# Kernel optimization log

Hardware: AMD Instinct MI355X
Metric: run time of the kernel (lower is better)

The kernel has to match this reference:

```python
import jax, jax.numpy as jnp
import numpy as np
import math

V, D, H, NH, T, S = 50257, 1024, 1024, 16, 128, 4096
HD = D // NH


def setup_inputs() -> dict:
    key = jax.random.key(0)
    ks = jax.random.split(key, 24)
    sc = 0.02

    def n(k, shape, scale=sc):
        return jax.random.normal(k, shape, dtype=jnp.float32) * scale

    return {
        "sentence": jax.random.randint(ks[0], (S,), 0, V),
        "emb": n(ks[1], (V, D), 1.0),
        # attention projections, stored as (in, out) = W.T of torch Linear
        "Wq": n(ks[2], (D, D)), "bq": jnp.zeros((D,), jnp.float32),
        "Wk": n(ks[3], (D, D)), "bk": jnp.zeros((D,), jnp.float32),
        "Wv": n(ks[4], (D, D)), "bv": jnp.zeros((D,), jnp.float32),
        "Wo": n(ks[5], (D, D)), "bo": jnp.zeros((D,), jnp.float32),
        # LSTM gate linears: (D+H, H) each
        "Wf": n(ks[6], (D + H, H)), "bf": jnp.zeros((H,), jnp.float32),
        "Wi": n(ks[7], (D + H, H)), "bi": jnp.zeros((H,), jnp.float32),
        "Wu": n(ks[8], (D + H, H)), "bu": jnp.zeros((H,), jnp.float32),
        "Wg": n(ks[9], (D + H, H)), "bg": jnp.zeros((H,), jnp.float32),
        # tagger
        "Wt": n(ks[10], (H, T)), "bt": jnp.zeros((T,), jnp.float32),
    }


def _forward(sentence, emb, Wq, bq, Wk, bk, Wv, bv, Wo, bo,
             Wf, bf, Wi, bi, Wu, bu, Wg, bg, Wt, bt):
    s = sentence.shape[0]
    x = emb[sentence]                       # [S, D] embedding gather
    h = x[:, None, :]                       # [S, 1, D]  (seq, batch, embed)

    # Faithful to the torch code: scores contract over the BATCH axis
    # (view(seq, batch, heads, hd).transpose(1, 2) -> (seq, heads, batch, hd)).
    def proj(W, b):
        return (h @ W + b).reshape(s, 1, NH, HD).transpose(0, 2, 1, 3)  # [S,NH,1,HD]

    q, k, v = proj(Wq, bq), proj(Wk, bk), proj(Wv, bv)
    scores = jnp.einsum('shbd,shcd->shbc', q, k) / math.sqrt(HD)  # [S,NH,1,1]
    w = jax.nn.softmax(scores, axis=-1)     # dropout inactive (eval)
    attn = jnp.einsum('shbc,shcd->shbd', w, v)          # [S,NH,1,HD]
    attn = attn.transpose(0, 2, 1, 3).reshape(s, 1, D)  # [S,1,D]
    attn = (attn @ Wo + bo)[:, 0, :]                    # [S, D]

    # Fused-gate LSTM scan (math identical to 4 separate Linears)
    Wall = jnp.concatenate([Wf, Wi, Wu, Wg], axis=1)    # [D+H, 4H]
    ball = jnp.concatenate([bf, bi, bu, bg])            # [4H]

    def step(carry, xt):
        hx, cx = carry                                   # [H], [H]
        gates = jnp.concatenate([xt, hx]) @ Wall + ball  # [4H]
        f, i, g, o = jnp.split(gates, 4)
        f, i, o = jax.nn.sigmoid(f), jax.nn.sigmoid(i), jax.nn.sigmoid(o)
        g = jnp.tanh(g)
        cx = f * cx + i * g
        hx = o * jnp.tanh(cx)
        return (hx, cx), hx

    zero = jnp.zeros((H,), dtype=attn.dtype)
    _, outs = jax.lax.scan(step, (zero, zero), attn)     # [S, H]

    logits = outs @ Wt + bt                              # [S, T]
    return jax.nn.log_softmax(logits, axis=1)


def reference(sentence, emb, Wq, bq, Wk, bk, Wv, bv, Wo, bo,
              Wf, bf, Wi, bi, Wu, bu, Wg, bg, Wt, bt):
    return _forward(sentence, emb, Wq, bq, Wk, bk, Wv, bv, Wo, bo,
                    Wf, bf, Wi, bi, Wu, bu, Wg, bg, Wt, bt)
```

## Files before the change

kernel.cpp:

```cpp
#include <hip/hip_runtime.h>
#include <hip/hip_bf16.h>

#define S 4096
#define D 1024
#define H 1024
#define T 128
#define G4 4096

__global__ void k_init(unsigned long long* hcomm) {
    int i = blockIdx.x * 256 + threadIdx.x;
    if (i < H) {
        hcomm[i]     = 0xFFFFFFFFFFFFFFFFull;
        hcomm[H + i] = 0ull;
    }
}

__global__ void k_bvo(const float* __restrict__ Wo, const float* __restrict__ bv,
                      const float* __restrict__ bo, float* __restrict__ bvo) {
    int j = blockIdx.x * 256 + threadIdx.x;
    if (j >= D) return;
    float s = bo[j];
    for (int k = 0; k < D; ++k) s = fmaf(bv[k], Wo[k * D + j], s);
    bvo[j] = s;
}

__global__ void k_concat(const float* __restrict__ Wf, const float* __restrict__ Wi,
                         const float* __restrict__ Wu, const float* __restrict__ Wg,
                         const float* __restrict__ bf, const float* __restrict__ bi,
                         const float* __restrict__ bu, const float* __restrict__ bg,
                         float* __restrict__ Wx, float* __restrict__ ball) {
    int idx = blockIdx.x * 256 + threadIdx.x;
    int k = idx >> 12;
    int col = idx & 4095;
    int g = col >> 10;
    int j = col & 1023;
    const float* W = (g == 0) ? Wf : (g == 1) ? Wi : (g == 2) ? Wu : Wg;
    Wx[idx] = W[k * D + j];
    if (idx < G4) {
        const float* b = (g == 0) ? bf : (g == 1) ? bi : (g == 2) ? bu : bg;
        ball[idx] = b[j];
    }
}

__global__ void __launch_bounds__(256) k_gemm128(
        const float* __restrict__ A, const float* __restrict__ B,
        const float* __restrict__ bias, const int* __restrict__ gidx,
        float* __restrict__ C, int M, int N, int K) {
    __shared__ float As[16][128];
    __shared__ float Bs[16][128];
    const int tid = threadIdx.x;
    const int bm = blockIdx.y * 128, bn = blockIdx.x * 128;

    const int wave = tid >> 6, lane = tid & 63;
    const int wr = wave >> 1, wc = wave & 1;
    const int lr = lane >> 3, lc = lane & 7;
    const int row0 = wr * 64 + lr * 8;
    const int col0 = wc * 64 + lc * 8;

    const int ra = tid >> 1;
    const int ca = (tid & 1) * 8;
    const int rb = tid >> 4;
    const int cb = (tid & 15) * 8;

    const long grow = gidx ? (long)gidx[bm + ra] : (long)(bm + ra);
    const float* Ap = A + (size_t)grow * K;
    const float* Bp = B + (size_t)bn + cb;

    float acc[8][8] = {};

    for (int kt = 0; kt < K; kt += 16) {
        float4 a0 = *reinterpret_cast<const float4*>(Ap + kt + ca);
        float4 a1 = *reinterpret_cast<const float4*>(Ap + kt + ca + 4);
        float4 bv0 = *reinterpret_cast<const float4*>(Bp + (size_t)(kt + rb) * N);
        float4 bv1 = *reinterpret_cast<const float4*>(Bp + (size_t)(kt + rb) * N + 4);
        As[ca + 0][ra] = a0.x; As[ca + 1][ra] = a0.y;
        As[ca + 2][ra] = a0.z; As[ca + 3][ra] = a0.w;
        As[ca + 4][ra] = a1.x; As[ca + 5][ra] = a1.y;
        As[ca + 6][ra] = a1.z; As[ca + 7][ra] = a1.w;
        *reinterpret_cast<float4*>(&Bs[rb][cb])     = bv0;
        *reinterpret_cast<float4*>(&Bs[rb][cb + 4]) = bv1;
        __syncthreads();
#pragma unroll
        for (int kk = 0; kk < 16; ++kk) {
            float a[8], b[8];
            *reinterpret_cast<float4*>(a)     = *reinterpret_cast<const float4*>(&As[kk][row0]);
            *reinterpret_cast<float4*>(a + 4) = *reinterpret_cast<const float4*>(&As[kk][row0 + 4]);
            *reinterpret_cast<float4*>(b)     = *reinterpret_cast<const float4*>(&Bs[kk][col0]);
            *reinterpret_cast<float4*>(b + 4) = *reinterpret_cast<const float4*>(&Bs[kk][col0 + 4]);
#pragma unroll
            for (int i = 0; i < 8; ++i)
#pragma unroll
                for (int j = 0; j < 8; ++j)
                    acc[i][j] = fmaf(a[i], b[j], acc[i][j]);
        }
        __syncthreads();
    }

    float bb[8];
#pragma unroll
    for (int j = 0; j < 8; ++j) bb[j] = bias ? bias[bn + col0 + j] : 0.f;

#pragma unroll
    for (int i = 0; i < 8; ++i) {
        float* Cp = C + (size_t)(bm + row0 + i) * N + bn + col0;
        float4 v0, v1;
        v0.x = acc[i][0] + bb[0]; v0.y = acc[i][1] + bb[1];
        v0.z = acc[i][2] + bb[2]; v0.w = acc[i][3] + bb[3];
        v1.x = acc[i][4] + bb[4]; v1.y = acc[i][5] + bb[5];
        v1.z = acc[i][6] + bb[6]; v1.w = acc[i][7] + bb[7];
        *reinterpret_cast<float4*>(Cp)     = v0;
        *reinterpret_cast<float4*>(Cp + 4) = v1;
    }
}

__global__ void __launch_bounds__(1024, 4) k_lstm(
        const float* __restrict__ Wf, const float* __restrict__ Wi,
        const float* __restrict__ Wu, const float* __restrict__ Wg,
        const float* __restrict__ P, float* __restrict__ outs,
        unsigned long long* __restrict__ hcomm) {
    __shared__ float hx_lds[H];
    const int tid = threadIdx.x;
    const int wg = blockIdx.x;
    const int wave = tid >> 6;
    const int lane = tid & 63;
    const int g = lane >> 4;
    const int r = lane & 15;
    const int j = wg * 16 + wave;

    const float* Wsel = (g == 0) ? Wf : (g == 1) ? Wi : (g == 2) ? Wu : Wg;

    float wreg[64];
#pragma unroll
    for (int m = 0; m < 64; ++m)
        wreg[m] = Wsel[(size_t)(H + r + 16 * m) * D + j];

    float cx = 0.f;
    float pcur = (r == 0) ? P[(size_t)g * H + j] : 0.f;
    float pnext = 0.f;

    for (int t = 0; t < S; ++t) {
        {
            const unsigned long long want = (unsigned long long)t;
            const int slot_r = (t - 1) & 1;
            unsigned long long v;
            do {
                v = __hip_atomic_load(&hcomm[(size_t)slot_r * H + tid],
                                      __ATOMIC_RELAXED, __HIP_MEMORY_SCOPE_AGENT);
            } while ((v >> 32) != want);
            hx_lds[tid] = __uint_as_float((unsigned int)v);
        }
        __syncthreads();

        float s0 = 0.f, s1 = 0.f, s2 = 0.f, s3 = 0.f;
#pragma unroll
        for (int m = 0; m < 64; m += 4) {
            s0 = fmaf(wreg[m + 0], hx_lds[r + 16 * (m + 0)], s0);
            s1 = fmaf(wreg[m + 1], hx_lds[r + 16 * (m + 1)], s1);
            s2 = fmaf(wreg[m + 2], hx_lds[r + 16 * (m + 2)], s2);
            s3 = fmaf(wreg[m + 3], hx_lds[r + 16 * (m + 3)], s3);
        }
        float s = (s0 + s1) + (s2 + s3);

        s += __shfl_xor(s, 1);
        s += __shfl_xor(s, 2);
        s += __shfl_xor(s, 4);
        s += __shfl_xor(s, 8);
        if (r == 0) s += pcur;

        float fg = __shfl(s, 0);
        float ig = __shfl(s, 16);
        float gg = __shfl(s, 32);
        float og = __shfl(s, 48);

        float f_ = 1.f / (1.f + __expf(-fg));
        float i_ = 1.f / (1.f + __expf(-ig));
        float g_ = tanhf(gg);
        float o_ = 1.f / (1.f + __expf(-og));
        cx = f_ * cx + i_ * g_;
        float h = o_ * tanhf(cx);

        if (lane == 0) {
            unsigned long long pk = ((unsigned long long)(t + 1) << 32) |
                                    (unsigned long long)__float_as_uint(h);
            __hip_atomic_store(&hcomm[(size_t)(t & 1) * H + j], pk,
                               __ATOMIC_RELAXED, __HIP_MEMORY_SCOPE_AGENT);
            outs[(size_t)t * H + j] = h;
        }

        if (r == 0 && t + 1 < S)
            pnext = P[(size_t)(t + 1) * G4 + g * H + j];

        __syncthreads();
        pcur = pnext;
    }
}

__global__ void __launch_bounds__(128) k_logits(
        const float* __restrict__ outs, const float* __restrict__ Wt,
        const float* __restrict__ bt, float* __restrict__ out) {
    __shared__ float row[H];
    __shared__ float red[2];
    int srow = blockIdx.x;
    int t = threadIdx.x;
    for (int i = t; i < H; i += 128) row[i] = outs[(size_t)srow * H + i];
    __syncthreads();

    float acc = bt[t];
    for (int k = 0; k < H; ++k) acc = fmaf(row[k], Wt[k * T + t], acc);

    float m = acc;
#pragma unroll
    for (int d = 1; d < 64; d <<= 1) m = fmaxf(m, __shfl_xor(m, d));
    if ((t & 63) == 0) red[t >> 6] = m;
    __syncthreads();
    m = fmaxf(red[0], red[1]);

    float e = __expf(acc - m);
    float sum = e;
#pragma unroll
    for (int d = 1; d < 64; d <<= 1) sum += __shfl_xor(sum, d);
    if ((t & 63) == 0) red[t >> 6] = sum;
    __syncthreads();
    sum = red[0] + red[1];

    out[(size_t)srow * T + t] = (acc - m) - logf(sum);
}

extern "C" void kernel_launch(void* const* d_in, const int* in_sizes, int n_in,
                              void* d_out, int out_size, void* d_ws, size_t ws_size,
                              hipStream_t stream) {
    (void)in_sizes; (void)n_in; (void)out_size; (void)ws_size;

    const int*   sentence = (const int*)  d_in[0];
    const float* emb      = (const float*)d_in[1];
    const float* Wv = (const float*)d_in[6];
    const float* bv = (const float*)d_in[7];
    const float* Wo = (const float*)d_in[8];
    const float* bo = (const float*)d_in[9];
    const float* Wf = (const float*)d_in[10];
    const float* bf = (const float*)d_in[11];
    const float* Wi = (const float*)d_in[12];
    const float* bi = (const float*)d_in[13];
    const float* Wu = (const float*)d_in[14];
    const float* bu = (const float*)d_in[15];
    const float* Wg = (const float*)d_in[16];
    const float* bg = (const float*)d_in[17];
    const float* Wt = (const float*)d_in[18];
    const float* bt = (const float*)d_in[19];
    float* out = (float*)d_out;

    float* ws    = (float*)d_ws;
    float* W_vo  = ws;
    float* Wx    = W_vo + 1024 * 1024;
    float* attn  = Wx   + 1024 * 4096;
    float* P     = attn + 4096 * 1024;
    float* outs  = P    + (size_t)4096 * 4096;
    float* bvo   = outs + 4096 * 1024;
    float* ball  = bvo  + 1024;
    unsigned long long* hcomm = (unsigned long long*)(ball + 4096);

    k_init<<<4, 256, 0, stream>>>(hcomm);
    k_bvo<<<4, 256, 0, stream>>>(Wo, bv, bo, bvo);
    k_concat<<<(1024 * 4096) / 256, 256, 0, stream>>>(Wf, Wi, Wu, Wg,
                                                      bf, bi, bu, bg, Wx, ball);

    k_gemm128<<<dim3(8, 8), 256, 0, stream>>>(Wv, Wo, nullptr, nullptr,
                                              W_vo, 1024, 1024, 1024);
    k_gemm128<<<dim3(8, 32), 256, 0, stream>>>(emb, W_vo, bvo, sentence,
                                               attn, 4096, 1024, 1024);
    k_gemm128<<<dim3(32, 32), 256, 0, stream>>>(attn, Wx, ball, nullptr,
                                                P, 4096, 4096, 1024);

    {
        void* args[] = { (void*)&Wf, (void*)&Wi, (void*)&Wu, (void*)&Wg,
                         (void*)&P, (void*)&outs, (void*)&hcomm };
        hipLaunchCooperativeKernel((void*)k_lstm, dim3(64), dim3(1024),
                                   args, 0, stream);
    }

    k_logits<<<4096, 128, 0, stream>>>(outs, Wt, bt, out);
}
```

Before: 11.47 ms.

## Relay LSTM hidden-state polling through per-XCD leader and local mirror

```diff
diff --git a/kernel.cpp b/kernel.cpp
--- a/kernel.cpp
+++ b/kernel.cpp
@@ -7,12 +7,33 @@
 #define T 128
 #define G4 4096
 
-__global__ void k_init(unsigned long long* hcomm) {
+#define TAG_POISON 0xFFFFFFFFFFFFFFFFull
+
+__device__ __forceinline__ unsigned long long load_xcd(const unsigned long long* p) {
+    unsigned long long v;
+    asm volatile("global_load_dwordx2 %0, %1, off sc0\n\t"
+                 "s_waitcnt vmcnt(0)"
+                 : "=v"(v) : "v"(p) : "memory");
+    return v;
+}
+__device__ __forceinline__ void store_xcd(unsigned long long* p, unsigned long long v) {
+    asm volatile("global_store_dwordx2 %0, %1, off sc0"
+                 :: "v"(p), "v"(v) : "memory");
+}
+
+__global__ void k_init(unsigned long long* hcomm, unsigned long long* mirror,
+                       unsigned int* xcnt) {
     int i = blockIdx.x * 256 + threadIdx.x;
     if (i < H) {
-        hcomm[i]     = 0xFFFFFFFFFFFFFFFFull;
+        hcomm[i]     = TAG_POISON;
         hcomm[H + i] = 0ull;
     }
+    if (i < 8 * H) {
+        int x = i >> 10, e = i & 1023;
+        mirror[((size_t)x * 2 + 0) * H + e] = TAG_POISON;
+        mirror[((size_t)x * 2 + 1) * H + e] = 0ull;
+    }
+    if (i < 8) xcnt[i] = 0u;
 }
 
 __global__ void k_bvo(const float* __restrict__ Wo, const float* __restrict__ bv,
@@ -117,8 +138,11 @@
         const float* __restrict__ Wf, const float* __restrict__ Wi,
         const float* __restrict__ Wu, const float* __restrict__ Wg,
         const float* __restrict__ P, float* __restrict__ outs,
-        unsigned long long* __restrict__ hcomm) {
+        unsigned long long* __restrict__ hcomm,
+        unsigned long long* __restrict__ mirror,
+        unsigned int* __restrict__ xcnt) {
     __shared__ float hx_lds[H];
+    __shared__ int s_leader;
     const int tid = threadIdx.x;
     const int wg = blockIdx.x;
     const int wave = tid >> 6;
@@ -127,12 +151,20 @@
     const int r = lane & 15;
     const int j = wg * 16 + wave;
 
+    const int xcd = __builtin_amdgcn_s_getreg(20 | (31 << 11)) & 7;
+    if (tid == 0)
+        s_leader = (atomicAdd(&xcnt[xcd], 1u) == 0u) ? 1 : 0;
+
     const float* Wsel = (g == 0) ? Wf : (g == 1) ? Wi : (g == 2) ? Wu : Wg;
 
     float wreg[64];
 #pragma unroll
     for (int m = 0; m < 64; ++m)
         wreg[m] = Wsel[(size_t)(H + r + 16 * m) * D + j];
+
+    __syncthreads();
+    const bool leader = (s_leader != 0);
+    unsigned long long* mir = mirror + (size_t)xcd * 2 * H;
 
     float cx = 0.f;
     float pcur = (r == 0) ? P[(size_t)g * H + j] : 0.f;
@@ -143,10 +175,27 @@
             const unsigned long long want = (unsigned long long)t;
             const int slot_r = (t - 1) & 1;
             unsigned long long v;
-            do {
-                v = __hip_atomic_load(&hcomm[(size_t)slot_r * H + tid],
-                                      __ATOMIC_RELAXED, __HIP_MEMORY_SCOPE_AGENT);
-            } while ((v >> 32) != want);
+            if (leader) {
+                do {
+                    v = __hip_atomic_load(&hcomm[(size_t)slot_r * H + tid],
+                                          __ATOMIC_RELAXED, __HIP_MEMORY_SCOPE_AGENT);
+                } while ((v >> 32) != want);
+                store_xcd(&mir[(size_t)slot_r * H + tid], v);
+            } else {
+                unsigned long long* mp = &mir[(size_t)slot_r * H + tid];
+                for (;;) {
+                    bool hit = false;
+#pragma unroll 1
+                    for (int q = 0; q < 32; ++q) {
+                        v = load_xcd(mp);
+                        if ((v >> 32) == want) { hit = true; break; }
+                    }
+                    if (hit) break;
+                    v = __hip_atomic_load(&hcomm[(size_t)slot_r * H + tid],
+                                          __ATOMIC_RELAXED, __HIP_MEMORY_SCOPE_AGENT);
+                    if ((v >> 32) == want) break;
+                }
+            }
             hx_lds[tid] = __uint_as_float((unsigned int)v);
         }
         __syncthreads();
@@ -257,9 +306,11 @@
     float* outs  = P    + (size_t)4096 * 4096;
     float* bvo   = outs + 4096 * 1024;
     float* ball  = bvo  + 1024;
-    unsigned long long* hcomm = (unsigned long long*)(ball + 4096);
-
-    k_init<<<4, 256, 0, stream>>>(hcomm);
+    unsigned long long* hcomm  = (unsigned long long*)(ball + 4096);
+    unsigned long long* mirror = hcomm + 2 * H;
+    unsigned int*       xcnt   = (unsigned int*)(mirror + 16 * H);
+
+    k_init<<<32, 256, 0, stream>>>(hcomm, mirror, xcnt);
     k_bvo<<<4, 256, 0, stream>>>(Wo, bv, bo, bvo);
     k_concat<<<(1024 * 4096) / 256, 256, 0, stream>>>(Wf, Wi, Wu, Wg,
                                                       bf, bi, bu, bg, Wx, ball);
@@ -273,7 +324,8 @@
 
     {
         void* args[] = { (void*)&Wf, (void*)&Wi, (void*)&Wu, (void*)&Wg,
-                         (void*)&P, (void*)&outs, (void*)&hcomm };
+                         (void*)&P, (void*)&outs, (void*)&hcomm,
+                         (void*)&mirror, (void*)&xcnt };
         hipLaunchCooperativeKernel((void*)k_lstm, dim3(64), dim3(1024),
                                    args, 0, stream);
     }
```

Result: slower. 27.13 ms (+136.5%).

## Add relay workgroups that replicate LSTM hidden-state broadcast to reduce polling contention

Applied to the files above, without the earlier changes.

```diff
diff --git a/kernel.cpp b/kernel.cpp
--- a/kernel.cpp
+++ b/kernel.cpp
@@ -7,11 +7,21 @@
 #define T 128
 #define G4 4096
 
-__global__ void k_init(unsigned long long* hcomm) {
+#define TAG_POISON 0xFFFFFFFFFFFFFFFFull
+#define NREP 8
+#define NCOMPUTE 64
+#define REPELEM 128
+
+__global__ void k_init(unsigned long long* hcomm, unsigned long long* hrep) {
     int i = blockIdx.x * 256 + threadIdx.x;
     if (i < H) {
-        hcomm[i]     = 0xFFFFFFFFFFFFFFFFull;
+        hcomm[i]     = TAG_POISON;
         hcomm[H + i] = 0ull;
+    }
+    if (i < NREP * H) {
+        int x = i >> 10, e = i & 1023;
+        hrep[((size_t)x * 2 + 0) * H + e] = TAG_POISON;
+        hrep[((size_t)x * 2 + 1) * H + e] = 0ull;
     }
 }
 
@@ -117,10 +127,30 @@
         const float* __restrict__ Wf, const float* __restrict__ Wi,
         const float* __restrict__ Wu, const float* __restrict__ Wg,
         const float* __restrict__ P, float* __restrict__ outs,
-        unsigned long long* __restrict__ hcomm) {
-    __shared__ float hx_lds[H];
+        unsigned long long* __restrict__ hcomm,
+        unsigned long long* __restrict__ hrep) {
     const int tid = threadIdx.x;
     const int wg = blockIdx.x;
+
+    if (wg >= NCOMPUTE) {
+        if (tid >= REPELEM) return;
+        const int e = (wg - NCOMPUTE) * REPELEM + tid;
+        for (unsigned int tau = 1; tau <= (unsigned int)S; ++tau) {
+            const int slot = (tau - 1) & 1;
+            unsigned long long v;
+            do {
+                v = __hip_atomic_load(&hcomm[(size_t)slot * H + e],
+                                      __ATOMIC_RELAXED, __HIP_MEMORY_SCOPE_AGENT);
+            } while ((unsigned int)(v >> 32) != tau);
+#pragma unroll
+            for (int x = 0; x < NREP; ++x)
+                __hip_atomic_store(&hrep[((size_t)x * 2 + slot) * H + e], v,
+                                   __ATOMIC_RELAXED, __HIP_MEMORY_SCOPE_AGENT);
+        }
+        return;
+    }
+
+    __shared__ float hx_lds[H];
     const int wave = tid >> 6;
     const int lane = tid & 63;
     const int g = lane >> 4;
@@ -134,19 +164,31 @@
     for (int m = 0; m < 64; ++m)
         wreg[m] = Wsel[(size_t)(H + r + 16 * m) * D + j];
 
+    unsigned long long* myrep = hrep + (size_t)(wg & (NREP - 1)) * 2 * H;
+
     float cx = 0.f;
     float pcur = (r == 0) ? P[(size_t)g * H + j] : 0.f;
     float pnext = 0.f;
 
     for (int t = 0; t < S; ++t) {
         {
-            const unsigned long long want = (unsigned long long)t;
+            const unsigned int want = (unsigned int)t;
             const int slot_r = (t - 1) & 1;
+            unsigned long long* mp = &myrep[(size_t)slot_r * H + tid];
             unsigned long long v;
-            do {
+            for (;;) {
+                bool hit = false;
+#pragma unroll 1
+                for (int q = 0; q < 16; ++q) {
+                    v = __hip_atomic_load(mp, __ATOMIC_RELAXED,
+                                          __HIP_MEMORY_SCOPE_AGENT);
+                    if ((unsigned int)(v >> 32) == want) { hit = true; break; }
+                }
+                if (hit) break;
                 v = __hip_atomic_load(&hcomm[(size_t)slot_r * H + tid],
                                       __ATOMIC_RELAXED, __HIP_MEMORY_SCOPE_AGENT);
-            } while ((v >> 32) != want);
+                if ((unsigned int)(v >> 32) == want) break;
+            }
             hx_lds[tid] = __uint_as_float((unsigned int)v);
         }
         __syncthreads();
@@ -258,8 +300,9 @@
     float* bvo   = outs + 4096 * 1024;
     float* ball  = bvo  + 1024;
     unsigned long long* hcomm = (unsigned long long*)(ball + 4096);
-
-    k_init<<<4, 256, 0, stream>>>(hcomm);
+    unsigned long long* hrep  = hcomm + 2 * H;
+
+    k_init<<<32, 256, 0, stream>>>(hcomm, hrep);
     k_bvo<<<4, 256, 0, stream>>>(Wo, bv, bo, bvo);
     k_concat<<<(1024 * 4096) / 256, 256, 0, stream>>>(Wf, Wi, Wu, Wg,
                                                       bf, bi, bu, bg, Wx, ball);
@@ -273,9 +316,9 @@
 
     {
         void* args[] = { (void*)&Wf, (void*)&Wi, (void*)&Wu, (void*)&Wg,
-                         (void*)&P, (void*)&outs, (void*)&hcomm };
-        hipLaunchCooperativeKernel((void*)k_lstm, dim3(64), dim3(1024),
-                                   args, 0, stream);
+                         (void*)&P, (void*)&outs, (void*)&hcomm, (void*)&hrep };
+        hipLaunchCooperativeKernel((void*)k_lstm, dim3(NCOMPUTE + NREP),
+                                   dim3(1024), args, 0, stream);
     }
 
     k_logits<<<4096, 128, 0, stream>>>(outs, Wt, bt, out);
```

Measured after the change: 14.23 ms. 24.0% more time.
